# Optimization experiments

Hardware: AMD Instinct MI355X
Metric: run time of the kernel (lower is better)

The kernel has to match this reference:

```python
import math
import jax, jax.numpy as jnp
import numpy as np

B = 8
NUM_POINTS = 4096
LATENT = 512
HID = 512
AD = 128
R1, R2, R_ATT = 1.0, 1.5, 0.2
EPS = 1e-5
SQRT_D = math.sqrt(AD)


def _fibonacci_sphere_points(n, radius):
    if n <= 0:
        return np.zeros((0, 3), np.float32)
    i = np.arange(n, dtype=np.float32)
    phi = (1 + 5 ** 0.5) / 2
    theta = 2 * math.pi * i / phi
    z = 1.0 - 2.0 * (i + 0.5) / n
    r_xy = np.sqrt(np.maximum(1.0 - z * z, 0.0))
    return (radius * np.stack((r_xy * np.cos(theta), r_xy * np.sin(theta), z), axis=-1)).astype(np.float32)


def _make_template():
    n_shell = NUM_POINTS - 1
    area_ratio = R1 ** 2 / (R1 ** 2 + R2 ** 2)
    n1 = max(1, round(n_shell * area_ratio))
    n2 = n_shell - n1
    if n2 == 0:
        n1, n2 = n1 - 1, 1
    t1 = _fibonacci_sphere_points(n1, R1)
    t2 = _fibonacci_sphere_points(n2, R2)
    return jnp.asarray(np.concatenate([np.zeros((1, 3), np.float32), t1, t2], axis=0))


def setup_inputs() -> dict:
    key = jax.random.key(0)
    ks = iter(jax.random.split(key, 64))
    d = {}
    d['z'] = jax.random.normal(next(ks), (B, LATENT), jnp.float32)
    d['template'] = _make_template()
    d['wq'] = jax.random.normal(next(ks), (AD, 3), jnp.float32) * 0.1
    d['wk'] = jax.random.normal(next(ks), (AD, 3), jnp.float32) * 0.1
    d['wv'] = jax.random.normal(next(ks), (AD, 3), jnp.float32) * 0.1
    in_dims = [LATENT + 3, LATENT + 3 + AD, LATENT + 3 + AD]
    for s, in_dim in enumerate(in_dims):
        d[f's{s}_w1'] = jax.random.normal(next(ks), (HID, in_dim), jnp.float32) * (1.0 / math.sqrt(in_dim))
        d[f's{s}_b1'] = jnp.zeros((HID,), jnp.float32)
        d[f's{s}_g1'] = jnp.ones((HID,), jnp.float32)
        d[f's{s}_be1'] = jnp.zeros((HID,), jnp.float32)
        d[f's{s}_w2'] = jax.random.normal(next(ks), (HID, HID), jnp.float32) * (1.0 / math.sqrt(HID))
        d[f's{s}_b2'] = jnp.zeros((HID,), jnp.float32)
        d[f's{s}_g2'] = jnp.ones((HID,), jnp.float32)
        d[f's{s}_be2'] = jnp.zeros((HID,), jnp.float32)
        d[f's{s}_w3'] = jax.random.normal(next(ks), (3, HID), jnp.float32) * (1.0 / math.sqrt(HID))
        d[f's{s}_b3'] = jnp.zeros((3,), jnp.float32)
    return d


def _bn_relu(x, gamma, beta):
    # BatchNorm1d in training mode over channel dim of (B, N, C): stats over (B, N)
    mean = jnp.mean(x, axis=(0, 1))
    var = jnp.var(x, axis=(0, 1))
    xn = (x - mean) * jax.lax.rsqrt(var + EPS)
    return jax.nn.relu(xn * gamma + beta)


def _stage(x, w1, b1, g1, be1, w2, b2, g2, be2, w3, b3):
    h = _bn_relu(x @ w1.T + b1, g1, be1)
    h = _bn_relu(h @ w2.T + b2, g2, be2)
    return h @ w3.T + b3


def _local_attention(coords, wq, wk, wv):
    Q = coords @ wq.T  # (B, N, AD)
    K = coords @ wk.T
    V = coords @ wv.T
    sq = jnp.sum(coords * coords, axis=-1)  # (B, N)
    D2 = sq[:, :, None] + sq[:, None, :] - 2.0 * jnp.einsum('bnd,bmd->bnm', coords, coords)
    mask = D2 <= R_ATT ** 2  # diagonal always True (D2=0)
    scores = jnp.einsum('bnd,bmd->bnm', Q, K) / SQRT_D
    scores = jnp.where(mask, scores, -jnp.inf)
    W = jax.nn.softmax(scores, axis=-1)
    W = jnp.where(mask, W, 0.0)
    return jnp.einsum('bnm,bmd->bnd', W, V)


def reference(z, template, wq, wk, wv,
              s0_w1, s0_b1, s0_g1, s0_be1, s0_w2, s0_b2, s0_g2, s0_be2, s0_w3, s0_b3,
              s1_w1, s1_b1, s1_g1, s1_be1, s1_w2, s1_b2, s1_g2, s1_be2, s1_w3, s1_b3,
              s2_w1, s2_b1, s2_g1, s2_be1, s2_w2, s2_b2, s2_g2, s2_be2, s2_w3, s2_b3):
    Bz = z.shape[0]
    z_exp = jnp.broadcast_to(z[:, None, :], (Bz, NUM_POINTS, LATENT))
    tmpl = jnp.broadcast_to(template[None], (Bz, NUM_POINTS, 3))
    coords0 = _stage(jnp.concatenate((z_exp, tmpl), axis=-1),
                     s0_w1, s0_b1, s0_g1, s0_be1, s0_w2, s0_b2, s0_g2, s0_be2, s0_w3, s0_b3)
    attn1 = _local_attention(coords0, wq, wk, wv)
    coords1 = _stage(jnp.concatenate((z_exp, coords0, attn1), axis=-1),
                     s1_w1, s1_b1, s1_g1, s1_be1, s1_w2, s1_b2, s1_g2, s1_be2, s1_w3, s1_b3)
    attn2 = _local_attention(coords1, wq, wk, wv)
    coords2 = _stage(jnp.concatenate((z_exp, coords1, attn2), axis=-1),
                     s2_w1, s2_b1, s2_g1, s2_be1, s2_w2, s2_b2, s2_g2, s2_be2, s2_w3, s2_b3)
    return coords2
```

## Files before the change

kernel.cpp:

```cpp
#include <hip/hip_runtime.h>
#include <math.h>

#define NPTS 4096
#define BATCH 8
#define HIDD 512
#define ROWS 32768
#define R_ATT2 0.04f
#define INV_SQRT_D 0.08838834764831845f
#define LOG2E 1.4426950408889634f

typedef unsigned short u16;
typedef unsigned int u32;
typedef __attribute__((ext_vector_type(8))) short s8v;
typedef __attribute__((ext_vector_type(4))) float f4v;

__device__ __forceinline__ float u2f(u16 v) { return __uint_as_float(((u32)v) << 16); }
__device__ __forceinline__ u16 f2u(float f) {
  u32 u = __float_as_uint(f);
  return (u16)((u + 0x7fffu + ((u >> 16) & 1u)) >> 16);
}
__device__ __forceinline__ u32 packtrunc(float x0, float x1) {
  return (__float_as_uint(x1) & 0xFFFF0000u) | (__float_as_uint(x0) >> 16);
}
__device__ __forceinline__ float fast_exp2(float x) {
  float r;
  asm("v_exp_f32 %0, %1" : "=v"(r) : "v"(x));
  return r;
}

__global__ void gram_k(const float* __restrict__ wq, const float* __restrict__ wk,
                       float* __restrict__ G) {
  int ab = threadIdx.x;
  if (ab < 9) {
    int a = ab / 3, b = ab % 3;
    float s = 0.f;
    for (int d = 0; d < 128; ++d) s = fmaf(wq[d * 3 + a], wk[d * 3 + b], s);
    G[ab] = s;
  }
}

__global__ __launch_bounds__(256) void prep2_k(
    const float* __restrict__ z, const float* __restrict__ w1, int ldw,
    const float* __restrict__ b1, const float* __restrict__ w2,
    float* __restrict__ zwbuf, float* __restrict__ ubuf,
    u16* __restrict__ w1abf, u16* __restrict__ w2bf, int doW1a) {
  int wid = blockIdx.x * 4 + (threadIdx.x >> 6);
  int lane = threadIdx.x & 63;
  {
    int b = wid >> 9, c = wid & 511;
    const float* zr = z + b * 512;
    const float* wr = w1 + (size_t)c * ldw;
    float acc = 0.f;
#pragma unroll
    for (int k = lane; k < 512; k += 64) acc = fmaf(zr[k], wr[k], acc);
#pragma unroll
    for (int off = 32; off; off >>= 1) acc += __shfl_down(acc, off);
    if (lane == 0) zwbuf[wid] = acc + b1[c];
  }
  int idx = blockIdx.x * 256 + threadIdx.x;
  if (idx < 1536) {
    int a = idx >> 9, c = idx & 511;
    ubuf[idx] = w1[(size_t)c * ldw + 512 + a];
  }
  if (doW1a && idx < 65536) {
    int n = idx >> 7, k = idx & 127;
    w1abf[idx] = f2u(w1[(size_t)n * 643 + 515 + k]);
  }
  w2bf[idx] = f2u(w2[idx]);
}

__global__ __launch_bounds__(256) void s0l1s_k(const float* __restrict__ tmpl,
                                               const float* __restrict__ u,
                                               const float* __restrict__ zw,
                                               u16* __restrict__ h,
                                               float* __restrict__ psum,
                                               float* __restrict__ psumsq) {
  __shared__ float Ls[4][512];
  __shared__ float Lq[4][512];
  int g = blockIdx.x;
  int wave = threadIdx.x >> 6, lane = threadIdx.x & 63;
  int b = g >> 8;
  int c0 = lane * 8;
  const float* zr = zw + b * 512 + c0;
  const float* u0 = u + c0;
  const float* u1 = u + 512 + c0;
  const float* u2 = u + 1024 + c0;
  float zv[8], u0v[8], u1v[8], u2v[8];
#pragma unroll
  for (int j = 0; j < 8; ++j) {
    zv[j] = zr[j]; u0v[j] = u0[j]; u1v[j] = u1[j]; u2v[j] = u2[j];
  }
  float s[8] = {0, 0, 0, 0, 0, 0, 0, 0}, q[8] = {0, 0, 0, 0, 0, 0, 0, 0};
  int row0 = g * 16 + wave * 4;
#pragma unroll
  for (int t = 0; t < 4; ++t) {
    int row = row0 + t;
    int n = row & (NPTS - 1);
    float tx = tmpl[n * 3], ty = tmpl[n * 3 + 1], tz = tmpl[n * 3 + 2];
    u32 outw[4];
#pragma unroll
    for (int jj = 0; jj < 4; ++jj) {
      float v0 = zv[2 * jj] + tx * u0v[2 * jj] + ty * u1v[2 * jj] + tz * u2v[2 * jj];
      float v1 = zv[2 * jj + 1] + tx * u0v[2 * jj + 1] + ty * u1v[2 * jj + 1] + tz * u2v[2 * jj + 1];
      outw[jj] = packtrunc(v0, v1);
      float r0 = u2f((u16)(outw[jj] & 0xffffu));
      float r1 = u2f((u16)(outw[jj] >> 16));
      s[2 * jj] += r0;     q[2 * jj] = fmaf(r0, r0, q[2 * jj]);
      s[2 * jj + 1] += r1; q[2 * jj + 1] = fmaf(r1, r1, q[2 * jj + 1]);
    }
    *(uint4*)(h + (size_t)row * 512 + c0) = *(const uint4*)outw;
  }
#pragma unroll
  for (int j = 0; j < 8; ++j) {
    Ls[wave][c0 + j] = s[j];
    Lq[wave][c0 + j] = q[j];
  }
  __syncthreads();
  int c2 = threadIdx.x * 2;
#pragma unroll
  for (int cc = 0; cc < 2; ++cc) {
    int c = c2 + cc;
    psum[g * 512 + c] = Ls[0][c] + Ls[1][c] + Ls[2][c] + Ls[3][c];
    psumsq[g * 512 + c] = Lq[0][c] + Lq[1][c] + Lq[2][c] + Lq[3][c];
  }
}

__global__ __launch_bounds__(256) void bnrelu_k(u16* __restrict__ h,
                                                const float* __restrict__ sc,
                                                const float* __restrict__ sh) {
  int nthreads = gridDim.x * 256;
  int total = ROWS * 512 / 8;
  for (int i = blockIdx.x * 256 + threadIdx.x; i < total; i += nthreads) {
    int k0 = (i * 8) & 511;
    uint4 v = *(const uint4*)(h + (size_t)i * 8);
    const u16* p = (const u16*)&v;
    u32 outw[4];
#pragma unroll
    for (int t = 0; t < 4; ++t) {
      float x0 = fmaxf(fmaf(u2f(p[2 * t]), sc[k0 + 2 * t], sh[k0 + 2 * t]), 0.f);
      float x1 = fmaxf(fmaf(u2f(p[2 * t + 1]), sc[k0 + 2 * t + 1], sh[k0 + 2 * t + 1]), 0.f);
      outw[t] = packtrunc(x0, x1);
    }
    *(uint4*)(h + (size_t)i * 8) = *(const uint4*)outw;
  }
}

template <bool MODE1>
__global__ __launch_bounds__(256) void gemm_mfma_k(
    const u16* __restrict__ A, int lda, const u16* __restrict__ B, int ldb, int K,
    const float* __restrict__ bias, const float* __restrict__ zw,
    const float* __restrict__ u, const float4* __restrict__ c4,
    u16* __restrict__ C, float* __restrict__ psum, float* __restrict__ psumsq) {
  __shared__ u16 As[128 * 32];
  __shared__ u16 Bs[128 * 32];
  int tid = threadIdx.x;
  int wave = tid >> 6, lane = tid & 63;
  int quad = lane >> 4, l16 = lane & 15;
  int m0 = blockIdx.x * 128, n0 = blockIdx.y * 128;
  int wm = (wave & 1) * 64, wn = (wave >> 1) * 64;
  int srow0 = lane >> 2;
  int sc8 = (lane & 3) * 8;
  f4v acc[4][4];
#pragma unroll
  for (int mi = 0; mi < 4; ++mi)
#pragma unroll
    for (int ni = 0; ni < 4; ++ni) acc[mi][ni] = (f4v){0.f, 0.f, 0.f, 0.f};

  for (int k0 = 0; k0 < K; k0 += 32) {
#pragma unroll
    for (int j = 0; j < 2; ++j) {
      int chunk = wave * 2 + j;
      int row = chunk * 16 + srow0;
      const u16* gA = A + (size_t)(m0 + row) * lda + k0 + sc8;
      const u16* gB = B + (size_t)(n0 + row) * ldb + k0 + sc8;
      __builtin_amdgcn_global_load_lds(
          (const __attribute__((address_space(1))) void*)gA,
          (__attribute__((address_space(3))) void*)(As + chunk * 512), 16, 0, 0);
      __builtin_amdgcn_global_load_lds(
          (const __attribute__((address_space(1))) void*)gB,
          (__attribute__((address_space(3))) void*)(Bs + chunk * 512), 16, 0, 0);
    }
    __syncthreads();
    s8v af[4], bfv[4];
#pragma unroll
    for (int mi = 0; mi < 4; ++mi)
      af[mi] = *(const s8v*)&As[(wm + mi * 16 + l16) * 32 + quad * 8];
#pragma unroll
    for (int ni = 0; ni < 4; ++ni)
      bfv[ni] = *(const s8v*)&Bs[(wn + ni * 16 + l16) * 32 + quad * 8];
#pragma unroll
    for (int mi = 0; mi < 4; ++mi)
#pragma unroll
      for (int ni = 0; ni < 4; ++ni)
        acc[mi][ni] = __builtin_amdgcn_mfma_f32_16x16x32_bf16(
            af[mi], bfv[ni], acc[mi][ni], 0, 0, 0);
    __syncthreads();
  }

  int batch = m0 >> 12;
  float e0[4], e1[4], e2[4], e3[4];
  float ps[4] = {0, 0, 0, 0}, pq[4] = {0, 0, 0, 0};
#pragma unroll
  for (int ni = 0; ni < 4; ++ni) {
    int gn = n0 + wn + ni * 16 + l16;
    if (MODE1) {
      e0[ni] = zw[batch * 512 + gn];
      e1[ni] = u[gn];
      e2[ni] = u[512 + gn];
      e3[ni] = u[1024 + gn];
    } else {
      e0[ni] = bias[gn];
    }
  }
#pragma unroll
  for (int mi = 0; mi < 4; ++mi) {
#pragma unroll
    for (int reg = 0; reg < 4; ++reg) {
      int gm = m0 + wm + mi * 16 + quad * 4 + reg;
      float cx = 0.f, cy = 0.f, cz = 0.f;
      if (MODE1) {
        float4 p = c4[gm];
        cx = p.x; cy = p.y; cz = p.z;
      }
#pragma unroll
      for (int ni = 0; ni < 4; ++ni) {
        int gn = n0 + wn + ni * 16 + l16;
        float v = acc[mi][ni][reg] + e0[ni];
        if (MODE1) v += cx * e1[ni] + cy * e2[ni] + cz * e3[ni];
        u16 r = f2u(v);
        C[(size_t)gm * 512 + gn] = r;
        float vr = u2f(r);
        ps[ni] += vr;
        pq[ni] = fmaf(vr, vr, pq[ni]);
      }
    }
  }
  float* Lps = (float*)As;
  float* Lpq = (float*)Bs;
#pragma unroll
  for (int ni = 0; ni < 4; ++ni) {
    Lps[((wave * 4 + quad) * 4 + ni) * 16 + l16] = ps[ni];
    Lpq[((wave * 4 + quad) * 4 + ni) * 16 + l16] = pq[ni];
  }
  __syncthreads();
  if (tid < 128) {
    int wn2 = tid >> 6, rem = tid & 63;
    int nni = rem >> 4, ll = rem & 15;
    int gn = n0 + wn2 * 64 + nni * 16 + ll;
    float s = 0.f, q = 0.f;
#pragma unroll
    for (int wv = 0; wv < 2; ++wv)
#pragma unroll
      for (int qd = 0; qd < 4; ++qd) {
        int w2 = wn2 * 2 + wv;
        s += Lps[((w2 * 4 + qd) * 4 + nni) * 16 + ll];
        q += Lpq[((w2 * 4 + qd) * 4 + nni) * 16 + ll];
      }
    psum[(size_t)blockIdx.x * 512 + gn] = s;
    psumsq[(size_t)blockIdx.x * 512 + gn] = q;
  }
}

__global__ __launch_bounds__(256) void bn_fin_k(
    const float* __restrict__ psum, const float* __restrict__ psumsq, int nslabs,
    const float* __restrict__ gamma, const float* __restrict__ beta,
    float* __restrict__ sc, float* __restrict__ sh) {
  int c = blockIdx.x * 4 + (threadIdx.x >> 6);
  int lane = threadIdx.x & 63;
  float s = 0.f, q = 0.f;
  for (int g = lane; g < nslabs; g += 64) {
    s += psum[g * 512 + c];
    q += psumsq[g * 512 + c];
  }
#pragma unroll
  for (int off = 32; off; off >>= 1) {
    s += __shfl_down(s, off);
    q += __shfl_down(q, off);
  }
  if (lane == 0) {
    float mean = s * (1.f / 32768.f);
    float var = fmaxf(q * (1.f / 32768.f) - mean * mean, 0.f);
    float inv = rsqrtf(var + 1e-5f);
    float scale = gamma[c] * inv;
    sc[c] = scale;
    sh[c] = beta[c] - mean * scale;
  }
}

__global__ __launch_bounds__(256) void l3_k(const u16* __restrict__ h,
                                            const float* __restrict__ sc,
                                            const float* __restrict__ sh,
                                            const float* __restrict__ w3,
                                            const float* __restrict__ b3,
                                            float4* __restrict__ c4out,
                                            float* __restrict__ fout) {
  int wid = blockIdx.x * 4 + (threadIdx.x >> 6);
  int lane = threadIdx.x & 63;
  int k0 = lane * 8;
  uint4 hv = *(const uint4*)(h + (size_t)wid * 512 + k0);
  const u16* hp = (const u16*)&hv;
  float a0 = 0, a1 = 0, a2 = 0;
#pragma unroll
  for (int j = 0; j < 8; ++j) {
    int k = k0 + j;
    float x = fmaxf(fmaf(u2f(hp[j]), sc[k], sh[k]), 0.f);
    a0 = fmaf(x, w3[k], a0);
    a1 = fmaf(x, w3[512 + k], a1);
    a2 = fmaf(x, w3[1024 + k], a2);
  }
#pragma unroll
  for (int off = 32; off; off >>= 1) {
    a0 += __shfl_down(a0, off);
    a1 += __shfl_down(a1, off);
    a2 += __shfl_down(a2, off);
  }
  if (lane == 0) {
    a0 += b3[0]; a1 += b3[1]; a2 += b3[2];
    if (c4out) {
      float sq = a0 * a0 + a1 * a1 + a2 * a2;
      c4out[wid] = make_float4(a0, a1, a2, sq);
    }
    if (fout) {
      fout[(size_t)wid * 3 + 0] = a0;
      fout[(size_t)wid * 3 + 1] = a1;
      fout[(size_t)wid * 3 + 2] = a2;
    }
  }
}

__global__ __launch_bounds__(256) void attn_k(const float4* __restrict__ c4,
                                              const float* __restrict__ G,
                                              const float* __restrict__ wv,
                                              u16* __restrict__ attnb) {
  int wave = threadIdx.x >> 6, lane = threadIdx.x & 63;
  int qbase = (blockIdx.x * 4 + wave) * 4;
  int b = qbase >> 12;
  const float4* cb = c4 + (size_t)b * NPTS;
  float cxq[4], cyq[4], czq[4], thrq[4], g0q[4], g1q[4], g2q[4];
#pragma unroll
  for (int q = 0; q < 4; ++q) {
    float4 cq = c4[qbase + q];
    cxq[q] = cq.x; cyq[q] = cq.y; czq[q] = cq.z;
    thrq[q] = 0.5f * (cq.w - R_ATT2);
    const float SC = INV_SQRT_D * LOG2E;
    g0q[q] = (cq.x * G[0] + cq.y * G[3] + cq.z * G[6]) * SC;
    g1q[q] = (cq.x * G[1] + cq.y * G[4] + cq.z * G[7]) * SC;
    g2q[q] = (cq.x * G[2] + cq.y * G[5] + cq.z * G[8]) * SC;
  }
  float swq[4] = {0, 0, 0, 0}, sxq[4] = {0, 0, 0, 0};
  float syq[4] = {0, 0, 0, 0}, szq[4] = {0, 0, 0, 0};

  float4 p = cb[lane];
  for (int m0 = 0; m0 < NPTS; m0 += 64) {
    float4 pn = cb[(m0 + 64 + lane) & (NPTS - 1)];
    float nhw = -0.5f * p.w;
#pragma unroll
    for (int q = 0; q < 4; ++q) {
      float dm = fmaf(cxq[q], p.x, fmaf(cyq[q], p.y, fmaf(czq[q], p.z, nhw)));
      float s2 = fmaf(g0q[q], p.x, fmaf(g1q[q], p.y, g2q[q] * p.z));
      float e = fast_exp2(s2);
      e = (dm >= thrq[q]) ? e : 0.f;
      swq[q] += e;
      sxq[q] = fmaf(e, p.x, sxq[q]);
      syq[q] = fmaf(e, p.y, syq[q]);
      szq[q] = fmaf(e, p.z, szq[q]);
    }
    p = pn;
  }
#pragma unroll
  for (int q = 0; q < 4; ++q) {
#pragma unroll
    for (int off = 32; off; off >>= 1) {
      swq[q] += __shfl_xor(swq[q], off);
      sxq[q] += __shfl_xor(sxq[q], off);
      syq[q] += __shfl_xor(syq[q], off);
      szq[q] += __shfl_xor(szq[q], off);
    }
  }
  int d0 = lane * 2;
  float w0 = wv[d0 * 3], w1 = wv[d0 * 3 + 1], w2 = wv[d0 * 3 + 2];
  float w3_ = wv[d0 * 3 + 3], w4 = wv[d0 * 3 + 4], w5 = wv[d0 * 3 + 5];
#pragma unroll
  for (int q = 0; q < 4; ++q) {
    float inv = 1.f / swq[q];
    float ox = sxq[q] * inv, oy = syq[q] * inv, oz = szq[q] * inv;
    float v0 = ox * w0 + oy * w1 + oz * w2;
    float v1 = ox * w3_ + oy * w4 + oz * w5;
    u32 pack = (u32)f2u(v0) | ((u32)f2u(v1) << 16);
    *(u32*)(attnb + (size_t)(qbase + q) * 128 + d0) = pack;
  }
}

extern "C" void kernel_launch(void* const* d_in, const int* in_sizes, int n_in,
                              void* d_out, int out_size, void* d_ws, size_t ws_size,
                              hipStream_t stream) {
  const float* z = (const float*)d_in[0];
  const float* tmpl = (const float*)d_in[1];
  const float* wq = (const float*)d_in[2];
  const float* wk = (const float*)d_in[3];
  const float* wv = (const float*)d_in[4];
  const float* sw[3][10];
  for (int s = 0; s < 3; ++s)
    for (int j = 0; j < 10; ++j) sw[s][j] = (const float*)d_in[5 + s * 10 + j];

  char* base = (char*)d_ws;
  size_t off = 0;
  auto alloc = [&](size_t bytes) -> void* {
    void* p = base + off;
    off = (off + bytes + 255) & ~(size_t)255;
    return p;
  };
  u16* hA = (u16*)alloc((size_t)ROWS * 512 * 2);
  u16* hB = (u16*)alloc((size_t)ROWS * 512 * 2);
  u16* attnb = (u16*)alloc((size_t)ROWS * 128 * 2);
  float4* c4 = (float4*)alloc((size_t)ROWS * 16);
  float* psum = (float*)alloc(2048 * 512 * 4);
  float* psumsq = (float*)alloc(2048 * 512 * 4);
  float* zwbuf = (float*)alloc(4096 * 4);
  float* scv = (float*)alloc(512 * 4);
  float* shv = (float*)alloc(512 * 4);
  float* G = (float*)alloc(256);
  u16* w1abf = (u16*)alloc(512 * 128 * 2);
  u16* w2bf = (u16*)alloc(512 * 512 * 2);
  float* ubuf = (float*)alloc(1536 * 4);

  gram_k<<<1, 64, 0, stream>>>(wq, wk, G);

  for (int s = 0; s < 3; ++s) {
    int ldw = (s == 0) ? 515 : 643;
    prep2_k<<<1024, 256, 0, stream>>>(z, sw[s][0], ldw, sw[s][1], sw[s][4],
                                      zwbuf, ubuf, w1abf, w2bf, s == 0 ? 0 : 1);
    if (s == 0) {
      s0l1s_k<<<2048, 256, 0, stream>>>(tmpl, ubuf, zwbuf, hA, psum, psumsq);
      bn_fin_k<<<128, 256, 0, stream>>>(psum, psumsq, 2048,
                                        sw[s][2], sw[s][3], scv, shv);
    } else {
      gemm_mfma_k<true><<<dim3(256, 4), 256, 0, stream>>>(
          attnb, 128, w1abf, 128, 128, nullptr, zwbuf, ubuf, c4,
          hA, psum, psumsq);
      bn_fin_k<<<128, 256, 0, stream>>>(psum, psumsq, 256,
                                        sw[s][2], sw[s][3], scv, shv);
    }
    bnrelu_k<<<2048, 256, 0, stream>>>(hA, scv, shv);
    gemm_mfma_k<false><<<dim3(256, 4), 256, 0, stream>>>(
        hA, 512, w2bf, 512, 512, sw[s][5], nullptr, nullptr, nullptr,
        hB, psum, psumsq);
    bn_fin_k<<<128, 256, 0, stream>>>(psum, psumsq, 256,
                                      sw[s][6], sw[s][7], scv, shv);
    bool last = (s == 2);
    l3_k<<<8192, 256, 0, stream>>>(hB, scv, shv, sw[s][8], sw[s][9],
                                   last ? nullptr : c4,
                                   last ? (float*)d_out : nullptr);
    if (!last) {
      attn_k<<<2048, 256, 0, stream>>>(c4, G, wv, attnb);
    }
  }
}
```

Baseline: 488.1 us.

## Compute local attention scores and weighted sums with bf16 split-precision MFMA

Replaces the scalar local-attention kernel with one that computes masked distance and score dot products via bf16 MFMA, using hi/lo bf16 splits to approximate fp32 accuracy. The exp weights are staged in LDS as bf16 and reduced against the coordinates with another MFMA. Each block now handles 64 queries, with 8 waves splitting the key range, and partial sums are combined in LDS. This targets the VALU-bound N^2 inner loop but adds LDS traffic, bf16 rounding of weights and coordinates in the weighted sum, and possible threshold-mask differences near the radius boundary.

```diff
diff --git a/kernel.cpp b/kernel.cpp
--- a/kernel.cpp
+++ b/kernel.cpp
@@ -13,6 +13,7 @@
 typedef unsigned int u32;
 typedef __attribute__((ext_vector_type(8))) short s8v;
 typedef __attribute__((ext_vector_type(4))) float f4v;
+typedef __attribute__((ext_vector_type(4))) u32 u4v;
 
 __device__ __forceinline__ float u2f(u16 v) { return __uint_as_float(((u32)v) << 16); }
 __device__ __forceinline__ u16 f2u(float f) {
@@ -26,6 +27,11 @@
   float r;
   asm("v_exp_f32 %0, %1" : "=v"(r) : "v"(x));
   return r;
+}
+__device__ __forceinline__ s8v mk8(u32 a, u32 b, u32 c, u32 d) {
+  union { u4v u; s8v s; } x;
+  x.u = (u4v){a, b, c, d};
+  return x.s;
 }
 
 __global__ void gram_k(const float* __restrict__ wq, const float* __restrict__ wk,
@@ -328,66 +334,146 @@
   }
 }
 
-__global__ __launch_bounds__(256) void attn_k(const float4* __restrict__ c4,
-                                              const float* __restrict__ G,
-                                              const float* __restrict__ wv,
-                                              u16* __restrict__ attnb) {
+__global__ __launch_bounds__(512) void attnm_k(const float4* __restrict__ c4,
+                                               const float* __restrict__ G,
+                                               const float* __restrict__ wv,
+                                               u16* __restrict__ attnb) {
+  __shared__ __align__(16) char lds[65536 + 4096 + 8192];
   int wave = threadIdx.x >> 6, lane = threadIdx.x & 63;
-  int qbase = (blockIdx.x * 4 + wave) * 4;
+  int g = lane >> 4, q16 = lane & 15;
+  int qbase = blockIdx.x * 64;
   int b = qbase >> 12;
   const float4* cb = c4 + (size_t)b * NPTS;
-  float cxq[4], cyq[4], czq[4], thrq[4], g0q[4], g1q[4], g2q[4];
-#pragma unroll
-  for (int q = 0; q < 4; ++q) {
-    float4 cq = c4[qbase + q];
-    cxq[q] = cq.x; cyq[q] = cq.y; czq[q] = cq.z;
-    thrq[q] = 0.5f * (cq.w - R_ATT2);
+  int pt0 = wave * 512;
+  char* ebufW = lds + wave * 8192;
+  char* ctW = lds + 65536 + wave * 512;
+  float* fin = (float*)(lds + 65536 + 4096);
+
+  float Gr[9];
+#pragma unroll
+  for (int i = 0; i < 9; ++i) Gr[i] = G[i];
+  u32 bh0[4], bh1[4], bh2[4], bh3[4];
+  u32 sh0[4], sh1[4], sh2[4], sh3[4];
+  float thr[4];
+#pragma unroll
+  for (int s = 0; s < 4; ++s) {
+    float4 cq = c4[qbase + s * 16 + q16];
+    thr[s] = 0.5f * (cq.w - R_ATT2);
+    u16 hx = f2u(cq.x), hy = f2u(cq.y), hz = f2u(cq.z);
+    u16 lx = f2u(cq.x - u2f(hx)), ly = f2u(cq.y - u2f(hy)), lz = f2u(cq.z - u2f(hz));
+    u32 h01 = (u32)hx | ((u32)hy << 16);
+    u32 h23 = (u32)hz | (0x3F80u << 16);
+    u32 l01 = (u32)lx | ((u32)ly << 16);
+    u32 l23 = (u32)lz;
+    bh0[s] = (g <= 1) ? h01 : 0u;
+    bh1[s] = (g <= 1) ? h23 : 0u;
+    bh2[s] = (g == 0) ? l01 : 0u;
+    bh3[s] = (g == 0) ? l23 : 0u;
     const float SC = INV_SQRT_D * LOG2E;
-    g0q[q] = (cq.x * G[0] + cq.y * G[3] + cq.z * G[6]) * SC;
-    g1q[q] = (cq.x * G[1] + cq.y * G[4] + cq.z * G[7]) * SC;
-    g2q[q] = (cq.x * G[2] + cq.y * G[5] + cq.z * G[8]) * SC;
-  }
-  float swq[4] = {0, 0, 0, 0}, sxq[4] = {0, 0, 0, 0};
-  float syq[4] = {0, 0, 0, 0}, szq[4] = {0, 0, 0, 0};
-
-  float4 p = cb[lane];
-  for (int m0 = 0; m0 < NPTS; m0 += 64) {
-    float4 pn = cb[(m0 + 64 + lane) & (NPTS - 1)];
-    float nhw = -0.5f * p.w;
-#pragma unroll
-    for (int q = 0; q < 4; ++q) {
-      float dm = fmaf(cxq[q], p.x, fmaf(cyq[q], p.y, fmaf(czq[q], p.z, nhw)));
-      float s2 = fmaf(g0q[q], p.x, fmaf(g1q[q], p.y, g2q[q] * p.z));
-      float e = fast_exp2(s2);
-      e = (dm >= thrq[q]) ? e : 0.f;
-      swq[q] += e;
-      sxq[q] = fmaf(e, p.x, sxq[q]);
-      syq[q] = fmaf(e, p.y, syq[q]);
-      szq[q] = fmaf(e, p.z, szq[q]);
-    }
-    p = pn;
-  }
-#pragma unroll
-  for (int q = 0; q < 4; ++q) {
-#pragma unroll
-    for (int off = 32; off; off >>= 1) {
-      swq[q] += __shfl_xor(swq[q], off);
-      sxq[q] += __shfl_xor(sxq[q], off);
-      syq[q] += __shfl_xor(syq[q], off);
-      szq[q] += __shfl_xor(szq[q], off);
-    }
-  }
-  int d0 = lane * 2;
-  float w0 = wv[d0 * 3], w1 = wv[d0 * 3 + 1], w2 = wv[d0 * 3 + 2];
-  float w3_ = wv[d0 * 3 + 3], w4 = wv[d0 * 3 + 4], w5 = wv[d0 * 3 + 5];
-#pragma unroll
-  for (int q = 0; q < 4; ++q) {
-    float inv = 1.f / swq[q];
-    float ox = sxq[q] * inv, oy = syq[q] * inv, oz = szq[q] * inv;
-    float v0 = ox * w0 + oy * w1 + oz * w2;
-    float v1 = ox * w3_ + oy * w4 + oz * w5;
+    float g0v = (cq.x * Gr[0] + cq.y * Gr[3] + cq.z * Gr[6]) * SC;
+    float g1v = (cq.x * Gr[1] + cq.y * Gr[4] + cq.z * Gr[7]) * SC;
+    float g2v = (cq.x * Gr[2] + cq.y * Gr[5] + cq.z * Gr[8]) * SC;
+    u16 ghx = f2u(g0v), ghy = f2u(g1v), ghz = f2u(g2v);
+    u16 glx = f2u(g0v - u2f(ghx)), gly = f2u(g1v - u2f(ghy)), glz = f2u(g2v - u2f(ghz));
+    u32 gh01 = (u32)ghx | ((u32)ghy << 16);
+    u32 gh23 = (u32)ghz;
+    u32 gl01 = (u32)glx | ((u32)gly << 16);
+    u32 gl23 = (u32)glz;
+    sh0[s] = (g <= 1) ? gh01 : 0u;
+    sh1[s] = (g <= 1) ? gh23 : 0u;
+    sh2[s] = (g == 0) ? gl01 : 0u;
+    sh3[s] = (g == 0) ? gl23 : 0u;
+  }
+
+  f4v pvAcc[4];
+#pragma unroll
+  for (int s = 0; s < 4; ++s) pvAcc[s] = (f4v){0.f, 0.f, 0.f, 0.f};
+
+  for (int w = 0; w < 16; ++w) {
+    int wpar = w & 1;
+    char* ebuf = ebufW + wpar * 4096;
+    char* ct = ctW + wpar * 256;
+#pragma unroll
+    for (int tp = 0; tp < 2; ++tp) {
+      int p = pt0 + w * 32 + tp * 16 + q16;
+      float4 pp = cb[p];
+      float nhw = -0.5f * pp.w;
+      u16 hx = f2u(pp.x), hy = f2u(pp.y), hz = f2u(pp.z), hw = f2u(nhw);
+      u16 lx = f2u(pp.x - u2f(hx)), ly = f2u(pp.y - u2f(hy));
+      u16 lz = f2u(pp.z - u2f(hz)), lw = f2u(nhw - u2f(hw));
+      u32 h01 = (u32)hx | ((u32)hy << 16), h23 = (u32)hz | ((u32)hw << 16);
+      u32 l01 = (u32)lx | ((u32)ly << 16), l23 = (u32)lz | ((u32)lw << 16);
+      u32 a0 = (g == 0) ? h01 : ((g == 1) ? l01 : 0u);
+      u32 a1 = (g == 0) ? h23 : ((g == 1) ? l23 : 0u);
+      u32 a2 = (g == 0) ? h01 : 0u;
+      u32 a3 = (g == 0) ? h23 : 0u;
+      s8v av = mk8(a0, a1, a2, a3);
+      if (g == 0) {
+        *(u16*)(ct + 64 + tp * 32 + q16 * 2) = hx;
+        *(u16*)(ct + 128 + tp * 32 + q16 * 2) = hy;
+        *(u16*)(ct + 192 + tp * 32 + q16 * 2) = hz;
+      }
+#pragma unroll
+      for (int s = 0; s < 4; ++s) {
+        f4v z4 = (f4v){0.f, 0.f, 0.f, 0.f};
+        f4v dmv = __builtin_amdgcn_mfma_f32_16x16x32_bf16(
+            av, mk8(bh0[s], bh1[s], bh2[s], bh3[s]), z4, 0, 0, 0);
+        f4v s2v = __builtin_amdgcn_mfma_f32_16x16x32_bf16(
+            av, mk8(sh0[s], sh1[s], sh2[s], sh3[s]), z4, 0, 0, 0);
+        float e0 = (dmv[0] >= thr[s]) ? fast_exp2(s2v[0]) : 0.f;
+        float e1 = (dmv[1] >= thr[s]) ? fast_exp2(s2v[1]) : 0.f;
+        float e2 = (dmv[2] >= thr[s]) ? fast_exp2(s2v[2]) : 0.f;
+        float e3 = (dmv[3] >= thr[s]) ? fast_exp2(s2v[3]) : 0.f;
+        u32* ew = (u32*)(ebuf + s * 1024 + q16 * 64 + tp * 32 + g * 8);
+        ew[0] = (u32)f2u(e0) | ((u32)f2u(e1) << 16);
+        ew[1] = (u32)f2u(e2) | ((u32)f2u(e3) << 16);
+      }
+    }
+    int cc = q16 & 3;
+    u4v bt = *(const u4v*)(ct + cc * 64 + g * 16);
+    if (q16 == 0) bt = (u4v){0x3F803F80u, 0x3F803F80u, 0x3F803F80u, 0x3F803F80u};
+    s8v pvB = mk8(bt.x, bt.y, bt.z, bt.w);
+#pragma unroll
+    for (int s = 0; s < 4; ++s) {
+      u4v at = *(const u4v*)(ebuf + s * 1024 + q16 * 64 + g * 16);
+      pvAcc[s] = __builtin_amdgcn_mfma_f32_16x16x32_bf16(
+          mk8(at.x, at.y, at.z, at.w), pvB, pvAcc[s], 0, 0, 0);
+    }
+  }
+
+  if (q16 < 4) {
+#pragma unroll
+    for (int s = 0; s < 4; ++s)
+#pragma unroll
+      for (int r = 0; r < 4; ++r)
+        fin[wave * 256 + (s * 16 + g * 4 + r) * 4 + q16] = pvAcc[s][r];
+  }
+  __syncthreads();
+  float* comb = (float*)lds;
+  int t = threadIdx.x;
+  if (t < 256) {
+    int qb = t >> 2, c = t & 3;
+    float acc = 0.f;
+#pragma unroll
+    for (int wv8 = 0; wv8 < 8; ++wv8) acc += fin[wv8 * 256 + qb * 4 + c];
+    comb[qb * 4 + c] = acc;
+  }
+  __syncthreads();
+#pragma unroll
+  for (int it = 0; it < 8; ++it) {
+    int task = t + it * 512;
+    int qb = task >> 6, dp = task & 63;
+    float sw = comb[qb * 4 + 0];
+    float sx = comb[qb * 4 + 1];
+    float sy = comb[qb * 4 + 2];
+    float sz = comb[qb * 4 + 3];
+    float inv = 1.f / sw;
+    float ox = sx * inv, oy = sy * inv, oz = sz * inv;
+    int d0 = dp * 2;
+    float v0 = ox * wv[d0 * 3] + oy * wv[d0 * 3 + 1] + oz * wv[d0 * 3 + 2];
+    float v1 = ox * wv[d0 * 3 + 3] + oy * wv[d0 * 3 + 4] + oz * wv[d0 * 3 + 5];
     u32 pack = (u32)f2u(v0) | ((u32)f2u(v1) << 16);
-    *(u32*)(attnb + (size_t)(qbase + q) * 128 + d0) = pack;
+    *(u32*)(attnb + (size_t)(qbase + qb) * 128 + d0) = pack;
   }
 }
 
@@ -452,7 +538,7 @@
                                    last ? nullptr : c4,
                                    last ? (float*)d_out : nullptr);
     if (!last) {
-      attn_k<<<2048, 256, 0, stream>>>(c4, G, wv, attnb);
-    }
-  }
-}
+      attnm_k<<<512, 512, 0, stream>>>(c4, G, wv, attnb);
+    }
+  }
+}
```

Measured after the change: 492.4 us. Within noise of the previous version (+0.9%).
